# Kernel optimization log

Measured on AMD Instinct MI355X. Metric: run time of the kernel, lower is better.

## Reference

```python
import jax, jax.numpy as jnp
import numpy as np

SIZE = 1024
N_HEAD = 16
HEAD_DIM = SIZE // N_HEAD


def setup_inputs() -> dict:
    key = jax.random.key(0)
    ks = jax.random.split(key, 5)
    s = 1.0 / np.sqrt(SIZE)
    return {
        "x": jax.random.normal(ks[0], (4, 2048, SIZE), dtype=jnp.float32),
        "w_qkv": jax.random.uniform(ks[1], (SIZE, 3 * SIZE), dtype=jnp.float32, minval=-s, maxval=s),
        "b_qkv": jax.random.uniform(ks[2], (3 * SIZE,), dtype=jnp.float32, minval=-s, maxval=s),
        "w_fc": jax.random.uniform(ks[3], (SIZE, SIZE), dtype=jnp.float32, minval=-s, maxval=s),
        "b_fc": jax.random.uniform(ks[4], (SIZE,), dtype=jnp.float32, minval=-s, maxval=s),
    }


def reference(x, w_qkv, b_qkv, w_fc, b_fc):
    B, S, D = x.shape
    qkv = x @ w_qkv + b_qkv                      # [B, S, 3D]
    qkv = qkv.reshape(B, S, 3, N_HEAD, HEAD_DIM)
    qkv = jnp.transpose(qkv, (2, 0, 3, 1, 4))    # [3, B, H, S, hd]
    q, k, v = qkv[0], qkv[1], qkv[2]
    scale = 1.0 / np.sqrt(HEAD_DIM).astype(np.float32)
    scores = jnp.einsum('bhqd,bhkd->bhqk', q, k) * scale
    attn = jax.nn.softmax(scores, axis=-1)
    out = jnp.einsum('bhqk,bhkd->bhqd', attn, v)  # [B, H, S, hd]
    out = jnp.transpose(out, (0, 2, 1, 3)).reshape(B, S, D)
    return out @ w_fc + b_fc
```

## Files before the change

kernel.cpp:

```cpp
#include <hip/hip_runtime.h>

#define DEV __device__ __forceinline__

typedef float  f32x4   __attribute__((ext_vector_type(4)));
typedef float  f32x16  __attribute__((ext_vector_type(16)));
typedef short  s16x4   __attribute__((ext_vector_type(4)));
typedef short  short8  __attribute__((ext_vector_type(8)));
typedef __bf16 bf16x8  __attribute__((ext_vector_type(8)));
typedef unsigned u32x2 __attribute__((ext_vector_type(2)));
typedef unsigned u32x4 __attribute__((ext_vector_type(4)));

DEV f32x4 mfma_bf16(short8 a, short8 b, f32x4 c) {
    return __builtin_amdgcn_mfma_f32_16x16x32_bf16(
        __builtin_bit_cast(bf16x8, a), __builtin_bit_cast(bf16x8, b), c, 0, 0, 0);
}

DEV f32x16 mfma32(short8 a, short8 b, f32x16 c) {
    return __builtin_amdgcn_mfma_f32_32x32x16_bf16(
        __builtin_bit_cast(bf16x8, a), __builtin_bit_cast(bf16x8, b), c, 0, 0, 0);
}

DEV void gload_lds16(const void* g, void* l) {
    __builtin_amdgcn_global_load_lds(
        (const __attribute__((address_space(1))) unsigned int*)g,
        (__attribute__((address_space(3))) unsigned int*)l, 16, 0, 0);
}

DEV short f2bf(float f) { return __builtin_bit_cast(short, (__bf16)f); }

DEV unsigned cvt_pk_bf16(float lo, float hi) {
    unsigned r;
    asm("v_cvt_pk_bf16_f32 %0, %1, %2" : "=v"(r) : "v"(lo), "v"(hi));
    return r;
}

DEV u32x2 pl32swap(unsigned a, unsigned b) {
    return __builtin_amdgcn_permlane32_swap(a, b, false, false);
}

DEV int xcd_swz(int fid, int nwg) {
    int cpx = nwg >> 3;
    return (fid & 7) * cpx + (fid >> 3);
}

__global__ void cast_x(const float* __restrict__ in, unsigned short* __restrict__ out, int n) {
    int i = (blockIdx.x * 256 + threadIdx.x) * 8;
    if (i >= n) return;
    f32x4 a = *(const f32x4*)(in + i);
    f32x4 b = *(const f32x4*)(in + i + 4);
    short8 o;
    o[0] = f2bf(a[0]); o[1] = f2bf(a[1]); o[2] = f2bf(a[2]); o[3] = f2bf(a[3]);
    o[4] = f2bf(b[0]); o[5] = f2bf(b[1]); o[6] = f2bf(b[2]); o[7] = f2bf(b[3]);
    *(short8*)(out + i) = o;
}

__global__ void transpose_cast(const float* __restrict__ in, unsigned short* __restrict__ out,
                               int R, int C) {
    __shared__ float tile[64][65];
    int c0 = blockIdx.x * 64, r0 = blockIdx.y * 64;
    int tx = threadIdx.x & 63, ty = threadIdx.x >> 6;
#pragma unroll
    for (int i = 0; i < 16; i++) {
        int r = i * 4 + ty;
        tile[r][tx] = in[(size_t)(r0 + r) * C + c0 + tx];
    }
    __syncthreads();
#pragma unroll
    for (int i = 0; i < 16; i++) {
        int cc = i * 4 + ty;
        out[(size_t)(c0 + cc) * R + r0 + tx] = (unsigned short)f2bf(tile[tx][cc]);
    }
}

template <int MODE>
__global__ __launch_bounds__(256, 2) void gemm_bt(
    const unsigned short* __restrict__ A, const unsigned short* __restrict__ Bt,
    const float* __restrict__ bias, float* __restrict__ out_f32,
    unsigned short* __restrict__ q_out, unsigned short* __restrict__ k_out,
    unsigned short* __restrict__ v_out, int K) {
    __shared__ __align__(16) char smem[32768];
    char* lA = smem;
    char* lB = smem + 16384;
    const int t = threadIdx.x;
    const int lane = t & 63, w = t >> 6;
    const int wr = w >> 1, wc = w & 1;
    const int nbx = gridDim.x;
    const int sw = xcd_swz(blockIdx.y * nbx + blockIdx.x, nbx * gridDim.y);
    const int rowBase = (sw / nbx) * 128, colBase = (sw % nbx) * 128;

    f32x4 acc[4][4] = {};

    for (int k0 = 0; k0 < K; k0 += 64) {
#pragma unroll
        for (int i = 0; i < 4; i++) {
            int c = i * 256 + t;
            int r = c >> 3, j = c & 7;
            int jj = j ^ (r & 7);
            gload_lds16(A  + (size_t)(rowBase + r) * K + k0 + jj * 8, lA + c * 16);
            gload_lds16(Bt + (size_t)(colBase + r) * K + k0 + jj * 8, lB + c * 16);
        }
        __syncthreads();
#pragma unroll
        for (int ks = 0; ks < 2; ks++) {
            const int colb = (ks * 4 + (lane >> 4)) * 16;
            short8 af[4], bfr[4];
#pragma unroll
            for (int m2 = 0; m2 < 4; m2++) {
                int r = wr * 64 + m2 * 16 + (lane & 15);
                af[m2] = *(const short8*)(lA + r * 128 + (colb ^ ((r & 7) << 4)));
            }
#pragma unroll
            for (int n2 = 0; n2 < 4; n2++) {
                int r = wc * 64 + n2 * 16 + (lane & 15);
                bfr[n2] = *(const short8*)(lB + r * 128 + (colb ^ ((r & 7) << 4)));
            }
            __builtin_amdgcn_s_setprio(1);
#pragma unroll
            for (int m2 = 0; m2 < 4; m2++)
#pragma unroll
                for (int n2 = 0; n2 < 4; n2++)
                    acc[m2][n2] = mfma_bf16(af[m2], bfr[n2], acc[m2][n2]);
            __builtin_amdgcn_s_setprio(0);
        }
        __syncthreads();
    }

    if (MODE == 0) {
        const int which = colBase >> 10;
        if (which == 2) {
#pragma unroll
            for (int n2 = 0; n2 < 4; n2++) {
                int gc = colBase + wc * 64 + n2 * 16 + (lane & 15);
                int rem = gc & 1023;
                int h = rem >> 6, d = rem & 63;
                float bv = bias[gc];
#pragma unroll
                for (int m2 = 0; m2 < 4; m2++) {
                    int grb = rowBase + wr * 64 + m2 * 16 + ((lane >> 4) << 2);
                    int b = grb >> 11, s = grb & 2047;
                    s16x4 o;
#pragma unroll
                    for (int r2 = 0; r2 < 4; r2++) o[r2] = f2bf(acc[m2][n2][r2] + bv);
                    *(s16x4*)(v_out + ((size_t)((b * 16 + h) * 64 + d)) * 2048 + s) = o;
                }
            }
        } else {
            const float qs = which == 0 ? 0.18033688011112042f : 1.0f;
            unsigned short* dst = which == 0 ? q_out : k_out;
#pragma unroll
            for (int n2 = 0; n2 < 4; n2++) {
                int gc = colBase + wc * 64 + n2 * 16 + (lane & 15);
                int rem = gc & 1023;
                int h = rem >> 6, d = rem & 63;
                float bv = bias[gc];
#pragma unroll
                for (int m2 = 0; m2 < 4; m2++) {
                    int grb = rowBase + wr * 64 + m2 * 16 + ((lane >> 4) << 2);
#pragma unroll
                    for (int r2 = 0; r2 < 4; r2++) {
                        int gr = grb + r2;
                        int b = gr >> 11, s = gr & 2047;
                        float v = (acc[m2][n2][r2] + bv) * qs;
                        dst[((size_t)((b * 16 + h) * 2048 + s)) * 64 + d] =
                            (unsigned short)f2bf(v);
                    }
                }
            }
        }
    } else {
#pragma unroll
        for (int n2 = 0; n2 < 4; n2++) {
            int gc = colBase + wc * 64 + n2 * 16 + (lane & 15);
            float bv = bias[gc];
#pragma unroll
            for (int m2 = 0; m2 < 4; m2++) {
                int grb = rowBase + wr * 64 + m2 * 16 + ((lane >> 4) << 2);
#pragma unroll
                for (int r2 = 0; r2 < 4; r2++)
                    out_f32[(size_t)(grb + r2) * 1024 + gc] = acc[m2][n2][r2] + bv;
            }
        }
    }
}

__global__ __launch_bounds__(256, 4) void fattn(
    const unsigned short* __restrict__ Qb, const unsigned short* __restrict__ Kb,
    const unsigned short* __restrict__ Vt, unsigned short* __restrict__ O) {
    __shared__ __align__(16) char smem[32768];
    const int t = threadIdx.x, lane = t & 63, w = t >> 6;
    const int h = lane >> 5, l5 = lane & 31;
    const int sw = xcd_swz(blockIdx.x, 1024);
    const int bh = sw >> 4;
    const int q0 = (sw & 15) * 128 + w * 32;
    const size_t slab = (size_t)bh * 2048 * 64;

    short8 qf[4];
#pragma unroll
    for (int s = 0; s < 4; s++)
        qf[s] = *(const short8*)(Qb + slab + (size_t)(q0 + l5) * 64 + s * 16 + h * 8);

#define STAGE_KV(kv0, buf)                                                          \
    do {                                                                            \
        char* dK_ = smem + (buf) * 8192;                                            \
        char* dV_ = smem + 16384 + (buf) * 8192;                                    \
        _Pragma("unroll")                                                           \
        for (int i_ = 0; i_ < 2; i_++) {                                            \
            int c_ = i_ * 256 + t, r_ = c_ >> 3, j_ = c_ & 7, jj_ = j_ ^ (r_ & 7);  \
            gload_lds16(Kb + slab + (size_t)((kv0) + r_) * 64 + jj_ * 8,            \
                        dK_ + c_ * 16);                                             \
            gload_lds16(Vt + slab + (size_t)r_ * 2048 + (kv0) + jj_ * 8,            \
                        dV_ + c_ * 16);                                             \
        }                                                                           \
    } while (0)

    STAGE_KV(0, 0);

    f32x4 lsum4 = {};
    f32x16 accO0 = {}, accO1 = {};

    int cur = 0;
    for (int kt = 0; kt < 32; kt++) {
        __syncthreads();
        if (kt < 31) STAGE_KV((kt + 1) * 64, cur ^ 1);
        char* lKc = smem + cur * 8192;
        char* lVc = smem + 16384 + cur * 8192;

        f32x16 st0 = {}, st1 = {};
        __builtin_amdgcn_s_setprio(1);
#pragma unroll
        for (int s = 0; s < 4; s++) {
            const int cb = s * 32 + h * 16;
            short8 k0 = *(const short8*)(lKc + l5 * 128 + (cb ^ ((l5 & 7) << 4)));
            short8 k1 = *(const short8*)(lKc + (32 + l5) * 128 + (cb ^ ((l5 & 7) << 4)));
            st0 = mfma32(k0, qf[s], st0);
            st1 = mfma32(k1, qf[s], st1);
        }
        __builtin_amdgcn_s_setprio(0);

#pragma unroll
        for (int kv2 = 0; kv2 < 2; kv2++) {
            const f32x16 stc = kv2 ? st1 : st0;
            unsigned pk[8];
#pragma unroll
            for (int i = 0; i < 8; i++) {
                float p0 = __builtin_amdgcn_exp2f(stc[2 * i]);
                float p1 = __builtin_amdgcn_exp2f(stc[2 * i + 1]);
                lsum4[i & 3] += p0 + p1;
                pk[i] = cvt_pk_bf16(p0, p1);
            }
            u32x2 s02 = pl32swap(pk[0], pk[2]);
            u32x2 s13 = pl32swap(pk[1], pk[3]);
            u32x2 s46 = pl32swap(pk[4], pk[6]);
            u32x2 s57 = pl32swap(pk[5], pk[7]);
            u32x4 af0 = {s02[0], s13[0], s02[1], s13[1]};
            u32x4 af1 = {s46[0], s57[0], s46[1], s57[1]};
            __builtin_amdgcn_s_setprio(1);
#pragma unroll
            for (int s = 0; s < 2; s++) {
                short8 ap = __builtin_bit_cast(short8, s == 0 ? af0 : af1);
                const int cb = kv2 * 64 + s * 32 + h * 16;
                short8 v0 = *(const short8*)(lVc + l5 * 128 + (cb ^ ((l5 & 7) << 4)));
                short8 v1 = *(const short8*)(lVc + (32 + l5) * 128 + (cb ^ ((l5 & 7) << 4)));
                accO0 = mfma32(ap, v0, accO0);
                accO1 = mfma32(ap, v1, accO1);
            }
            __builtin_amdgcn_s_setprio(0);
        }
        cur ^= 1;
    }
#undef STAGE_KV

    float lsum = lsum4[0] + lsum4[1] + lsum4[2] + lsum4[3];
    lsum += __shfl_xor(lsum, 32);
    float inv = 1.f / lsum;

    const int b = bh >> 4, hh = bh & 15;
#pragma unroll
    for (int r = 0; r < 16; r++) {
        int row = (r & 3) + 8 * (r >> 2) + 4 * h;
        float iv = __shfl(inv, row, 64);
        size_t base = ((size_t)(b * 2048 + q0 + row)) * 1024 + hh * 64;
        O[base + l5]      = (unsigned short)f2bf(accO0[r] * iv);
        O[base + 32 + l5] = (unsigned short)f2bf(accO1[r] * iv);
    }
}

extern "C" void kernel_launch(void* const* d_in, const int* in_sizes, int n_in,
                              void* d_out, int out_size, void* d_ws, size_t ws_size,
                              hipStream_t stream) {
    const float* x     = (const float*)d_in[0];
    const float* w_qkv = (const float*)d_in[1];
    const float* b_qkv = (const float*)d_in[2];
    const float* w_fc  = (const float*)d_in[3];
    const float* b_fc  = (const float*)d_in[4];

    char* ws = (char*)d_ws;
    unsigned short* Xb    = (unsigned short*)(ws);
    unsigned short* WqkvT = (unsigned short*)(ws + 16777216);
    unsigned short* WfcT  = (unsigned short*)(ws + 23068672);
    unsigned short* Qb    = (unsigned short*)(ws + 25165824);
    unsigned short* Kb    = (unsigned short*)(ws + 41943040);
    unsigned short* Vt    = (unsigned short*)(ws + 58720256);
    unsigned short* Ao    = (unsigned short*)(ws + 75497472);

    cast_x<<<dim3(8388608 / (256 * 8)), 256, 0, stream>>>(x, Xb, 8388608);
    transpose_cast<<<dim3(3072 / 64, 1024 / 64), 256, 0, stream>>>(w_qkv, WqkvT, 1024, 3072);
    transpose_cast<<<dim3(1024 / 64, 1024 / 64), 256, 0, stream>>>(w_fc, WfcT, 1024, 1024);

    gemm_bt<0><<<dim3(3072 / 128, 8192 / 128), 256, 0, stream>>>(
        Xb, WqkvT, b_qkv, nullptr, Qb, Kb, Vt, 1024);

    fattn<<<dim3(1024), 256, 0, stream>>>(Qb, Kb, Vt, Ao);

    gemm_bt<1><<<dim3(1024 / 128, 8192 / 128), 256, 0, stream>>>(
        Ao, WfcT, b_fc, (float*)d_out, nullptr, nullptr, nullptr, 1024);
}
```

Measured before the change: 257.8 us.

## Double-buffer GEMM LDS tiles and merge weight transpose launches

The GEMM now keeps two LDS buffers and issues the global-to-LDS loads for the next K tile before computing on the current one, so memory latency overlaps the MFMA work. This also drops one barrier per iteration. The two weight transpose-cast kernels are merged into a single launch to save launch overhead. LDS use doubles to 64KB per block, which with launch_bounds(256,2) may lower occupancy.

```diff
diff --git a/kernel.cpp b/kernel.cpp
--- a/kernel.cpp
+++ b/kernel.cpp
@@ -54,10 +54,23 @@
     *(short8*)(out + i) = o;
 }
 
-__global__ void transpose_cast(const float* __restrict__ in, unsigned short* __restrict__ out,
-                               int R, int C) {
+__global__ void transpose_cast2(const float* __restrict__ wqkv, unsigned short* __restrict__ oq,
+                                const float* __restrict__ wfc, unsigned short* __restrict__ of) {
     __shared__ float tile[64][65];
-    int c0 = blockIdx.x * 64, r0 = blockIdx.y * 64;
+    int bid = blockIdx.x;
+    const float* in;
+    unsigned short* out;
+    int bx, by, C;
+    if (bid < 48 * 16) {
+        in = wqkv; out = oq; C = 3072;
+        bx = bid % 48; by = bid / 48;
+    } else {
+        bid -= 48 * 16;
+        in = wfc; out = of; C = 1024;
+        bx = bid % 16; by = bid / 16;
+    }
+    const int R = 1024;
+    int c0 = bx * 64, r0 = by * 64;
     int tx = threadIdx.x & 63, ty = threadIdx.x >> 6;
 #pragma unroll
     for (int i = 0; i < 16; i++) {
@@ -78,9 +91,7 @@
     const float* __restrict__ bias, float* __restrict__ out_f32,
     unsigned short* __restrict__ q_out, unsigned short* __restrict__ k_out,
     unsigned short* __restrict__ v_out, int K) {
-    __shared__ __align__(16) char smem[32768];
-    char* lA = smem;
-    char* lB = smem + 16384;
+    __shared__ __align__(16) char smem[65536];
     const int t = threadIdx.x;
     const int lane = t & 63, w = t >> 6;
     const int wr = w >> 1, wc = w & 1;
@@ -88,18 +99,32 @@
     const int sw = xcd_swz(blockIdx.y * nbx + blockIdx.x, nbx * gridDim.y);
     const int rowBase = (sw / nbx) * 128, colBase = (sw % nbx) * 128;
 
+#define STAGE_AB(k0, buf)                                                           \
+    do {                                                                            \
+        char* lA_ = smem + (buf) * 32768;                                           \
+        char* lB_ = lA_ + 16384;                                                    \
+        _Pragma("unroll")                                                           \
+        for (int i_ = 0; i_ < 4; i_++) {                                            \
+            int c_ = i_ * 256 + t;                                                  \
+            int r_ = c_ >> 3, j_ = c_ & 7;                                          \
+            int jj_ = j_ ^ (r_ & 7);                                                \
+            gload_lds16(A  + (size_t)(rowBase + r_) * K + (k0) + jj_ * 8,           \
+                        lA_ + c_ * 16);                                             \
+            gload_lds16(Bt + (size_t)(colBase + r_) * K + (k0) + jj_ * 8,           \
+                        lB_ + c_ * 16);                                             \
+        }                                                                           \
+    } while (0)
+
+    STAGE_AB(0, 0);
+
     f32x4 acc[4][4] = {};
+    int cur = 0;
 
     for (int k0 = 0; k0 < K; k0 += 64) {
-#pragma unroll
-        for (int i = 0; i < 4; i++) {
-            int c = i * 256 + t;
-            int r = c >> 3, j = c & 7;
-            int jj = j ^ (r & 7);
-            gload_lds16(A  + (size_t)(rowBase + r) * K + k0 + jj * 8, lA + c * 16);
-            gload_lds16(Bt + (size_t)(colBase + r) * K + k0 + jj * 8, lB + c * 16);
-        }
         __syncthreads();
+        if (k0 + 64 < K) STAGE_AB(k0 + 64, cur ^ 1);
+        char* lA = smem + cur * 32768;
+        char* lB = lA + 16384;
 #pragma unroll
         for (int ks = 0; ks < 2; ks++) {
             const int colb = (ks * 4 + (lane >> 4)) * 16;
@@ -122,8 +147,9 @@
                     acc[m2][n2] = mfma_bf16(af[m2], bfr[n2], acc[m2][n2]);
             __builtin_amdgcn_s_setprio(0);
         }
-        __syncthreads();
-    }
+        cur ^= 1;
+    }
+#undef STAGE_AB
 
     if (MODE == 0) {
         const int which = colBase >> 10;
@@ -304,8 +330,7 @@
     unsigned short* Ao    = (unsigned short*)(ws + 75497472);
 
     cast_x<<<dim3(8388608 / (256 * 8)), 256, 0, stream>>>(x, Xb, 8388608);
-    transpose_cast<<<dim3(3072 / 64, 1024 / 64), 256, 0, stream>>>(w_qkv, WqkvT, 1024, 3072);
-    transpose_cast<<<dim3(1024 / 64, 1024 / 64), 256, 0, stream>>>(w_fc, WfcT, 1024, 1024);
+    transpose_cast2<<<dim3(48 * 16 + 16 * 16), 256, 0, stream>>>(w_qkv, WqkvT, w_fc, WfcT);
 
     gemm_bt<0><<<dim3(3072 / 128, 8192 / 128), 256, 0, stream>>>(
         Xb, WqkvT, b_qkv, nullptr, Qb, Kb, Vt, 1024);
```

Result: no change. 253.2 us (-1.8%).
